# Performance work log

Hardware: AMD Instinct MI355X
Metric: run time of the kernel (lower is better)

## Reference

```python
import jax, jax.numpy as jnp
import numpy as np

N_NODES = 50000
N_EDGES = 400000
LATENT = 128
HIDDEN = 512
N_HEADS = 2          # latent // 64, NodeAttn default num_heads
HEAD_DIM = LATENT // N_HEADS
N_GRAPHS = 500
LN_EPS = 1e-5


def setup_inputs() -> dict:
    key = jax.random.key(0)
    ks = jax.random.split(key, 24)
    s = 0.02
    inp = {
        "edges": jax.random.randint(ks[0], (2, N_EDGES), 0, N_NODES, dtype=jnp.int32),
        "node_feat": jax.random.normal(ks[1], (N_NODES, LATENT), jnp.float32),
        "edge_attr": jax.random.normal(ks[2], (N_EDGES, LATENT), jnp.float32),
        "u": jax.random.normal(ks[3], (N_GRAPHS, LATENT), jnp.float32),
        "num_nodes": jnp.full((N_GRAPHS,), N_NODES // N_GRAPHS, jnp.int32),
        # NodeAttn params (shared for sent/received calls, as in the module)
        "w1": jax.random.normal(ks[4], (3 * LATENT, LATENT), jnp.float32) * s,
        "b1": jnp.zeros((LATENT,), jnp.float32),
        "w2": jax.random.normal(ks[5], (N_HEADS, HEAD_DIM), jnp.float32) * s,
        "w3": jax.random.normal(ks[6], (2 * LATENT, LATENT), jnp.float32) * s,
        "b3": jnp.zeros((LATENT,), jnp.float32),
        # Encoder MLP: 4*latent -> hidden -> hidden -> latent, LN before ReLU
        "mw0": jax.random.normal(ks[7], (4 * LATENT, HIDDEN), jnp.float32) * s,
        "mb0": jnp.zeros((HIDDEN,), jnp.float32),
        "ls0": jnp.ones((HIDDEN,), jnp.float32),
        "lb0": jnp.zeros((HIDDEN,), jnp.float32),
        "mw1": jax.random.normal(ks[8], (HIDDEN, HIDDEN), jnp.float32) * s,
        "mb1": jnp.zeros((HIDDEN,), jnp.float32),
        "ls1": jnp.ones((HIDDEN,), jnp.float32),
        "lb1": jnp.zeros((HIDDEN,), jnp.float32),
        "mw2": jax.random.normal(ks[9], (HIDDEN, LATENT), jnp.float32) * s,
        "mb2": jnp.zeros((LATENT,), jnp.float32),
    }
    return inp


def _layer_norm(x, scale, bias):
    mu = jnp.mean(x, axis=-1, keepdims=True)
    var = jnp.mean(jnp.square(x - mu), axis=-1, keepdims=True)
    return (x - mu) * jax.lax.rsqrt(var + LN_EPS) * scale + bias


def _node_attn(q, k, ea, index, n_nodes, w1, b1, w2, w3, b3):
    # per-edge multi-head scores -> segment softmax over destination index -> scatter-add
    h = jax.nn.leaky_relu(jnp.concatenate([q, k, ea], axis=-1) @ w1 + b1, 0.2)
    h = h.reshape(-1, N_HEADS, HEAD_DIM)                    # [E, H, D]
    logits = jnp.einsum("ehd,hd->eh", h, w2)                 # [E, H]
    m = jax.ops.segment_max(logits, index, num_segments=n_nodes)
    m = jnp.where(jnp.isfinite(m), m, 0.0)                   # empty segments
    e = jnp.exp(logits - m[index])
    z = jax.ops.segment_sum(e, index, num_segments=n_nodes)
    alpha = e / (z[index] + 1e-16)                           # [E, H]
    v = (jnp.concatenate([k, ea], axis=-1) @ w3 + b3).reshape(-1, N_HEADS, HEAD_DIM)
    out = jax.ops.segment_sum(alpha[..., None] * v, index, num_segments=n_nodes)
    return out.reshape(n_nodes, LATENT)


def reference(edges, node_feat, edge_attr, u, num_nodes, w1, b1, w2, w3, b3,
              mw0, mb0, ls0, lb0, mw1, mb1, ls1, lb1, mw2, mb2):
    n = node_feat.shape[0]
    row, col = edges[0], edges[1]
    sent = _node_attn(node_feat[row], node_feat[col], edge_attr, row, n, w1, b1, w2, w3, b3)
    recv = _node_attn(node_feat[col], node_feat[row], edge_attr, col, n, w1, b1, w2, w3, b3)
    glob = jnp.repeat(u, num_nodes, axis=0, total_repeat_length=n)
    x = jnp.concatenate([node_feat, sent, recv, glob], axis=1)   # [N, 4*latent]
    h = jax.nn.relu(_layer_norm(x @ mw0 + mb0, ls0, lb0))
    h = jax.nn.relu(_layer_norm(h @ mw1 + mb1, ls1, lb1))
    return h @ mw2 + mb2
```

## Files before the change

### kernel.cpp

```cpp
#include <hip/hip_runtime.h>
#include <math.h>

#define LATENT 128

typedef __attribute__((ext_vector_type(8))) short bf16x8;
typedef __attribute__((ext_vector_type(4))) float f32x4;
typedef __attribute__((ext_vector_type(2))) float f32x2;
typedef __attribute__((ext_vector_type(2))) int i32x2;
typedef __attribute__((ext_vector_type(2))) unsigned u32x2;
typedef __attribute__((ext_vector_type(4))) unsigned u32x4;

union U4B { uint4 u; bf16x8 v; };

template <typename T>
__device__ __forceinline__ T ntl(const T* p) { return __builtin_nontemporal_load(p); }

__device__ __forceinline__ unsigned short f2bf(float f) {
    unsigned int x = __float_as_uint(f);
    unsigned int r = (x + 0x7fffu + ((x >> 16) & 1u)) >> 16;
    return (unsigned short)r;
}
__device__ __forceinline__ float bf2f(unsigned short h) {
    return __uint_as_float(((unsigned int)h) << 16);
}
__device__ __forceinline__ unsigned pk2(float a, float b) {
    return (unsigned)f2bf(a) | ((unsigned)f2bf(b) << 16);
}

__device__ __forceinline__ void gld16(const void* g, void* l) {
    __builtin_amdgcn_global_load_lds(
        (const __attribute__((address_space(1))) unsigned int*)g,
        (__attribute__((address_space(3))) unsigned int*)l, 16, 0, 0);
}

__global__ void k_gid(const int* __restrict__ num_nodes, int G, int n, int* __restrict__ gid) {
    __shared__ int goff[1025];
    if (threadIdx.x == 0) {
        int acc = 0;
        for (int g = 0; g < G; ++g) { goff[g] = acc; acc += num_nodes[g]; }
        goff[G] = acc;
    }
    __syncthreads();
    for (int g = 0; g < G; ++g) {
        int s = goff[g];
        int e = goff[g + 1]; if (e > n) e = n;
        for (int i = s + (int)threadIdx.x; i < e; i += blockDim.x) gid[i] = g;
    }
}

#define FN  1152
#define FE3 1248
#define FEV 1280
__global__ __launch_bounds__(256) void k_pack2(const float* __restrict__ mw0,
                                               const float* __restrict__ mw1,
                                               const float* __restrict__ mw2,
                                               const float* __restrict__ w1,
                                               const float* __restrict__ w3,
                                               uint4* __restrict__ pw) {
    int tid = blockIdx.x * 256 + threadIdx.x;
    if (tid >= 1312 * 64) return;
    int fid = tid >> 6, lane = tid & 63;
    const float* src; int kt, nt, N;
    if (fid < 512)       { src = mw0;            kt = fid >> 5;           nt = fid & 31;           N = 512; }
    else if (fid < 1024) { src = mw1;            kt = (fid - 512) >> 5;   nt = (fid - 512) & 31;   N = 512; }
    else if (fid < 1152) { src = mw2;            kt = (fid - 1024) >> 3;  nt = (fid - 1024) & 7;   N = 128; }
    else if (fid < 1184) { src = w1;             kt = (fid - 1152) >> 3;  nt = (fid - 1152) & 7;   N = 128; }
    else if (fid < 1216) { src = w1 + 128 * 128; kt = (fid - 1184) >> 3;  nt = (fid - 1184) & 7;   N = 128; }
    else if (fid < 1248) { src = w3;             kt = (fid - 1216) >> 3;  nt = (fid - 1216) & 7;   N = 128; }
    else if (fid < 1280) { src = w1 + 256 * 128; kt = (fid - 1248) >> 3;  nt = (fid - 1248) & 7;   N = 128; }
    else                 { src = w3 + 128 * 128; kt = (fid - 1280) >> 3;  nt = (fid - 1280) & 7;   N = 128; }
    int col = nt * 16 + (lane & 15);
    int k0 = kt * 32 + (lane >> 4) * 8;
    unsigned int w[4];
#pragma unroll
    for (int p = 0; p < 4; ++p) {
        unsigned int lo = f2bf(src[(size_t)(k0 + 2 * p) * N + col]);
        unsigned int hi = f2bf(src[(size_t)(k0 + 2 * p + 1) * N + col]);
        w[p] = lo | (hi << 16);
    }
    pw[(size_t)fid * 64 + lane] = make_uint4(w[0], w[1], w[2], w[3]);
}

__global__ void k_count(const int* __restrict__ edges, int E,
                        int* __restrict__ deg_s, int* __restrict__ deg_r) {
    int e = blockIdx.x * 256 + threadIdx.x;
    if (e < E) { atomicAdd(&deg_s[edges[e]], 1); atomicAdd(&deg_r[edges[E + e]], 1); }
}

__global__ __launch_bounds__(1024) void k_scan(const int* __restrict__ deg, int n,
                                               int* __restrict__ rowptr, int* __restrict__ cursor) {
    __shared__ int wsum[16];
    int t = threadIdx.x;
    int chunk = (n + 1023) / 1024;
    int s = t * chunk; if (s > n) s = n;
    int epos = s + chunk; if (epos > n) epos = n;
    int sum = 0;
    for (int i = s; i < epos; ++i) sum += deg[i];
    int lane = t & 63, wid = t >> 6;
    int v = sum;
#pragma unroll
    for (int d = 1; d < 64; d <<= 1) { int o = __shfl_up(v, d); if (lane >= d) v += o; }
    if (lane == 63) wsum[wid] = v;
    __syncthreads();
    if (t < 16) {
        int wv = wsum[t];
#pragma unroll
        for (int d = 1; d < 16; d <<= 1) { int o = __shfl_up(wv, d, 16); if (t >= d) wv += o; }
        wsum[t] = wv;
    }
    __syncthreads();
    int woff = wid ? wsum[wid - 1] : 0;
    int run = v + woff - sum;
    for (int i = s; i < epos; ++i) { rowptr[i] = run; cursor[i] = run; run += deg[i]; }
    if (t == 1023) rowptr[n] = run;
}

__global__ void k_fill(const int* __restrict__ edges, int E,
                       int* __restrict__ cur_s, int* __restrict__ cur_r,
                       int* __restrict__ os_s, int* __restrict__ os_r,
                       int* __restrict__ sm_s, int* __restrict__ sm_r) {
    int e = blockIdx.x * 256 + threadIdx.x;
    if (e < E) {
        int r = edges[e], c = edges[E + e];
        int p = atomicAdd(&cur_s[r], 1); os_s[p] = c; sm_s[e] = p;
        int q = atomicAdd(&cur_r[c], 1); os_r[q] = r; sm_r[e] = q;
    }
}

__global__ __launch_bounds__(512) void k_nodepre2(const float* __restrict__ nf, int n,
                                                  const uint4* __restrict__ pw,
                                                  unsigned short* __restrict__ PQK,
                                                  unsigned short* __restrict__ PVh) {
    __shared__ uint4 xs[32 * 64];
    int t = threadIdx.x, lane = t & 63, w = t >> 6;
    int wr = w >> 2, wc = w & 3, l15 = lane & 15, lg = lane >> 4;
    int base = blockIdx.x * 128;
#pragma unroll
    for (int it = 0; it < 4; ++it) {
        int chunk = t + it * 512;
        int row = chunk >> 4, k8 = chunk & 15, k = k8 * 8;
        int node = base + row;
        f32x4 v0 = (f32x4)(0.f), v1 = (f32x4)(0.f);
        if (node < n) {
            const f32x4* s4 = (const f32x4*)(nf + (size_t)node * 128 + k);
            v0 = ntl(s4); v1 = ntl(s4 + 1);
        }
        uint4 pkv;
        pkv.x = pk2(v0.x, v0.y); pkv.y = pk2(v0.z, v0.w);
        pkv.z = pk2(v1.x, v1.y); pkv.w = pk2(v1.z, v1.w);
        int kt = k >> 5, g = (k >> 3) & 3;
        xs[(kt * 8 + (row >> 4)) * 64 + g * 16 + (row & 15)] = pkv;
    }
    __syncthreads();
    f32x4 acc[4][6];
#pragma unroll
    for (int rt = 0; rt < 4; ++rt)
#pragma unroll
        for (int ct = 0; ct < 6; ++ct) acc[rt][ct] = (f32x4)(0.f);
    for (int kt = 0; kt < 4; ++kt) {
        U4B a[4];
#pragma unroll
        for (int rt = 0; rt < 4; ++rt) a[rt].u = xs[(kt * 8 + wr * 4 + rt) * 64 + lane];
        U4B b[6];
#pragma unroll
        for (int ct = 0; ct < 6; ++ct) {
            int nt = wc * 6 + ct;
            int mat = nt >> 3, ntm = nt & 7;
            b[ct].u = pw[(size_t)(FN + mat * 32 + kt * 8 + ntm) * 64 + lane];
        }
#pragma unroll
        for (int rt = 0; rt < 4; ++rt)
#pragma unroll
            for (int ct = 0; ct < 6; ++ct)
                acc[rt][ct] = __builtin_amdgcn_mfma_f32_16x16x32_bf16(a[rt].v, b[ct].v, acc[rt][ct], 0, 0, 0);
    }
#pragma unroll
    for (int rt = 0; rt < 4; ++rt)
#pragma unroll
        for (int ct = 0; ct < 6; ++ct) {
            int nt = wc * 6 + ct;
#pragma unroll
            for (int reg = 0; reg < 4; ++reg) {
                int node = base + (wr * 4 + rt) * 16 + lg * 4 + reg;
                if (node < n) {
                    unsigned short hv = f2bf(acc[rt][ct][reg]);
                    if (nt < 16) PQK[(size_t)node * 256 + nt * 16 + l15] = hv;
                    else         PVh[(size_t)node * 128 + (nt - 16) * 16 + l15] = hv;
                }
            }
        }
}

__global__ __launch_bounds__(256) void k_eproj1(const int* __restrict__ edges,
                                                const float* __restrict__ ea, int E,
                                                const uint4* __restrict__ pw,
                                                const unsigned short* __restrict__ PQK,
                                                const float* __restrict__ b1,
                                                const float* __restrict__ w2,
                                                const int* __restrict__ sm_s,
                                                const int* __restrict__ sm_r,
                                                unsigned short* __restrict__ EVs,
                                                unsigned short* __restrict__ EVr,
                                                float* __restrict__ ess2, float* __restrict__ ers2) {
    __shared__ uint4 xs[16 * 64];
    __shared__ unsigned short edata[64 * 128];
    __shared__ unsigned short evdata[64 * 128];
    int t = threadIdx.x, lane = t & 63, w = t >> 6;
    int wc = w, l15 = lane & 15, lg = lane >> 4;
    int base = blockIdx.x * 64;
#pragma unroll
    for (int it = 0; it < 4; ++it) {
        int chunk = t + it * 256;
        int row = chunk >> 4, k8 = chunk & 15, k = k8 * 8;
        int e = base + row;
        f32x4 v0 = (f32x4)(0.f), v1 = (f32x4)(0.f);
        if (e < E) {
            const f32x4* s4 = (const f32x4*)(ea + (size_t)e * 128 + k);
            v0 = ntl(s4); v1 = ntl(s4 + 1);
        }
        uint4 pkv;
        pkv.x = pk2(v0.x, v0.y); pkv.y = pk2(v0.z, v0.w);
        pkv.z = pk2(v1.x, v1.y); pkv.w = pk2(v1.z, v1.w);
        int kt = k >> 5, g = (k >> 3) & 3;
        xs[(kt * 4 + (row >> 4)) * 64 + g * 16 + (row & 15)] = pkv;
    }
    __syncthreads();
    f32x4 acc[4][4];
#pragma unroll
    for (int rt = 0; rt < 4; ++rt)
#pragma unroll
        for (int ct = 0; ct < 4; ++ct) acc[rt][ct] = (f32x4)(0.f);
    for (int kt = 0; kt < 4; ++kt) {
        U4B a[4];
#pragma unroll
        for (int rt = 0; rt < 4; ++rt) a[rt].u = xs[(kt * 4 + rt) * 64 + lane];
        U4B b[4];
        b[0].u = pw[(size_t)(FE3 + kt * 8 + wc * 2 + 0) * 64 + lane];
        b[1].u = pw[(size_t)(FE3 + kt * 8 + wc * 2 + 1) * 64 + lane];
        b[2].u = pw[(size_t)(FEV + kt * 8 + wc * 2 + 0) * 64 + lane];
        b[3].u = pw[(size_t)(FEV + kt * 8 + wc * 2 + 1) * 64 + lane];
#pragma unroll
        for (int rt = 0; rt < 4; ++rt)
#pragma unroll
            for (int ct = 0; ct < 4; ++ct)
                acc[rt][ct] = __builtin_amdgcn_mfma_f32_16x16x32_bf16(a[rt].v, b[ct].v, acc[rt][ct], 0, 0, 0);
    }
#pragma unroll
    for (int rt = 0; rt < 4; ++rt)
#pragma unroll
        for (int cc = 0; cc < 2; ++cc) {
            int col = (wc * 2 + cc) * 16 + l15;
#pragma unroll
            for (int reg = 0; reg < 4; ++reg) {
                int e_loc = rt * 16 + lg * 4 + reg;
                edata[e_loc * 128 + col]  = f2bf(acc[rt][cc][reg]);
                evdata[e_loc * 128 + col] = f2bf(acc[rt][2 + cc][reg]);
            }
        }
    __syncthreads();
    {
        int e4 = lane >> 4, piece = lane & 15;
#pragma unroll
        for (int i = 0; i < 4; ++i) {
            int e_loc = w * 16 + i * 4 + e4;
            int e = base + e_loc;
            if (e < E) {
                u32x4 v = *(const u32x4*)&evdata[e_loc * 128 + piece * 8];
                __builtin_nontemporal_store(v, (u32x4*)(EVs + (size_t)sm_s[e] * 128 + piece * 8));
                __builtin_nontemporal_store(v, (u32x4*)(EVr + (size_t)sm_r[e] * 128 + piece * 8));
            }
        }
    }
    int esub = lane >> 3, dg = lane & 7;
    float b1r[16], w2r[16];
    {
        const float4* b4 = (const float4*)(b1 + dg * 16);
        const float4* w4 = (const float4*)(w2 + (dg >> 2) * 64 + (dg & 3) * 16);
#pragma unroll
        for (int q = 0; q < 4; ++q) {
            float4 bv = b4[q], wv = w4[q];
            b1r[q * 4 + 0] = bv.x; b1r[q * 4 + 1] = bv.y; b1r[q * 4 + 2] = bv.z; b1r[q * 4 + 3] = bv.w;
            w2r[q * 4 + 0] = wv.x; w2r[q * 4 + 1] = wv.y; w2r[q * 4 + 2] = wv.z; w2r[q * 4 + 3] = wv.w;
        }
    }
#pragma unroll
    for (int it = 0; it < 2; ++it) {
        int e_loc = w * 16 + it * 8 + esub;
        int e = base + e_loc;
        if (e >= E) break;
        int r = edges[e], c = edges[E + e];
        const uint4* Aqr = (const uint4*)(PQK + ((size_t)r << 8) + dg * 16);
        const uint4* Akc = (const uint4*)(PQK + ((size_t)c << 8) + 128 + dg * 16);
        const uint4* Aqc = (const uint4*)(PQK + ((size_t)c << 8) + dg * 16);
        const uint4* Akr = (const uint4*)(PQK + ((size_t)r << 8) + 128 + dg * 16);
        const uint4* Ae3 = (const uint4*)(&edata[e_loc * 128 + dg * 16]);
        float ps = 0.f, pr = 0.f;
#pragma unroll
        for (int half = 0; half < 2; ++half) {
            uint4 uqr = Aqr[half], ukc = Akc[half], uqc = Aqc[half], ukr = Akr[half], ue3 = Ae3[half];
            unsigned wqr[4] = {uqr.x, uqr.y, uqr.z, uqr.w};
            unsigned wkc[4] = {ukc.x, ukc.y, ukc.z, ukc.w};
            unsigned wqc[4] = {uqc.x, uqc.y, uqc.z, uqc.w};
            unsigned wkr[4] = {ukr.x, ukr.y, ukr.z, ukr.w};
            unsigned we3[4] = {ue3.x, ue3.y, ue3.z, ue3.w};
#pragma unroll
            for (int q = 0; q < 4; ++q) {
#pragma unroll
                for (int hl = 0; hl < 2; ++hl) {
                    int i = half * 8 + q * 2 + hl;
                    float fqr = hl ? __uint_as_float(wqr[q] & 0xffff0000u) : __uint_as_float(wqr[q] << 16);
                    float fkc = hl ? __uint_as_float(wkc[q] & 0xffff0000u) : __uint_as_float(wkc[q] << 16);
                    float fqc = hl ? __uint_as_float(wqc[q] & 0xffff0000u) : __uint_as_float(wqc[q] << 16);
                    float fkr = hl ? __uint_as_float(wkr[q] & 0xffff0000u) : __uint_as_float(wkr[q] << 16);
                    float fe3 = hl ? __uint_as_float(we3[q] & 0xffff0000u) : __uint_as_float(we3[q] << 16);
                    float com = fe3 + b1r[i];
                    float hs = fqr + fkc + com; hs = hs > 0.f ? hs : 0.2f * hs;
                    float hr = fqc + fkr + com; hr = hr > 0.f ? hr : 0.2f * hr;
                    ps += hs * w2r[i]; pr += hr * w2r[i];
                }
            }
        }
        ps += __shfl_xor(ps, 1); ps += __shfl_xor(ps, 2);
        pr += __shfl_xor(pr, 1); pr += __shfl_xor(pr, 2);
        float Es = expf(ps), Er = expf(pr);
        if (dg == 0) {
            __builtin_nontemporal_store(Es, &ess2[(size_t)sm_s[e] * 2]);
            __builtin_nontemporal_store(Er, &ers2[(size_t)sm_r[e] * 2]);
        } else if (dg == 4) {
            __builtin_nontemporal_store(Es, &ess2[(size_t)sm_s[e] * 2 + 1]);
            __builtin_nontemporal_store(Er, &ers2[(size_t)sm_r[e] * 2 + 1]);
        }
    }
}

__global__ __launch_bounds__(256) void k_aggr(int n,
                                              const int* __restrict__ rps, const int* __restrict__ os_s,
                                              const int* __restrict__ rpr, const int* __restrict__ os_r,
                                              const float* __restrict__ ess2, const float* __restrict__ ers2,
                                              const unsigned short* __restrict__ PVh,
                                              const unsigned short* __restrict__ EVs,
                                              const unsigned short* __restrict__ EVr,
                                              const float* __restrict__ b3,
                                              unsigned short* __restrict__ out_sh,
                                              unsigned short* __restrict__ out_rh) {
    int w = threadIdx.x >> 6, lane = threadIdx.x & 63;
    int unit = blockIdx.x * 4 + w;
    if (unit >= 2 * n) return;
    bool sent = unit < n;
    int node = sent ? unit : unit - n;
    const int*   rp = sent ? rps : rpr;
    const int*   os = sent ? os_s : os_r;
    const float* ex = sent ? ess2 : ers2;
    const unsigned* EVx = (const unsigned*)(sent ? EVs : EVr);
    const unsigned* PV32 = (const unsigned*)PVh;
    int s0 = rp[node], s1 = rp[node + 1];
    float b3a = b3[2 * lane], b3b = b3[2 * lane + 1];
    float z0 = 0.f, z1 = 0.f, acca = 0.f, accb = 0.f;
    int j = s0;
    for (; j + 4 <= s1; j += 4) {
        int oth[4]; f32x2 ez[4]; unsigned ev[4], pv[4];
#pragma unroll
        for (int q = 0; q < 4; ++q) oth[q] = os[j + q];
#pragma unroll
        for (int q = 0; q < 4; ++q) ez[q] = ntl((const f32x2*)(ex + 2 * (j + q)));
#pragma unroll
        for (int q = 0; q < 4; ++q) ev[q] = ntl(EVx + (size_t)(j + q) * 64 + lane);
#pragma unroll
        for (int q = 0; q < 4; ++q) pv[q] = PV32[(size_t)oth[q] * 64 + lane];
#pragma unroll
        for (int q = 0; q < 4; ++q) {
            float va = __uint_as_float(ev[q] << 16) + __uint_as_float(pv[q] << 16) + b3a;
            float vb = __uint_as_float(ev[q] & 0xffff0000u) + __uint_as_float(pv[q] & 0xffff0000u) + b3b;
            z0 += ez[q].x; z1 += ez[q].y;
            float aw = (lane < 32) ? ez[q].x : ez[q].y;
            acca += aw * va; accb += aw * vb;
        }
    }
    for (; j < s1; ++j) {
        int oth = os[j];
        f32x2 ez = ntl((const f32x2*)(ex + 2 * j));
        unsigned ev = ntl(EVx + (size_t)j * 64 + lane);
        unsigned pv = PV32[(size_t)oth * 64 + lane];
        float va = __uint_as_float(ev << 16) + __uint_as_float(pv << 16) + b3a;
        float vb = __uint_as_float(ev & 0xffff0000u) + __uint_as_float(pv & 0xffff0000u) + b3b;
        z0 += ez.x; z1 += ez.y;
        float aw = (lane < 32) ? ez.x : ez.y;
        acca += aw * va; accb += aw * vb;
    }
    float zz = (lane < 32) ? z0 : z1;
    float rz = 1.f / (zz + 1e-16f);
    unsigned o = pk2(acca * rz, accb * rz);
    unsigned* outp = (unsigned*)(sent ? out_sh : out_rh);
    outp[(size_t)node * 64 + lane] = o;
}

__global__ __launch_bounds__(512) void k_mlp9(
    const float* __restrict__ nf, const unsigned short* __restrict__ out_sh,
    const unsigned short* __restrict__ out_rh,
    const float* __restrict__ u, const int* __restrict__ gid, int n,
    const uint4* __restrict__ pw,
    const float* __restrict__ mb0, const float* __restrict__ ls0, const float* __restrict__ lb0,
    const float* __restrict__ mb1, const float* __restrict__ ls1, const float* __restrict__ lb1,
    const float* __restrict__ mb2, float* __restrict__ out) {
    extern __shared__ char smem[];
    char* hx = smem;
    char* bb = smem + 65536;
    float2* red = (float2*)(smem + 131072);

    int t = threadIdx.x, lane = t & 63, w = t >> 6;
    int wr = w >> 2, wc = w & 3, l15 = lane & 15, lg = lane >> 4;
    int base = blockIdx.x * 64;

    auto stage32 = [&](int fragbase, int d) {
        const uint4* src = pw + (size_t)fragbase * 64;
        char* dst = bb + (size_t)d * 32768;
#pragma unroll
        for (int q = 0; q < 4; ++q)
            gld16(src + q * 512 + t, dst + ((size_t)q * 512 + t) * 16);
    };
    auto stage8 = [&](int fragbase, int d) {
        const uint4* src = pw + (size_t)fragbase * 64;
        char* dst = bb + (size_t)d * 32768;
        gld16(src + t, dst + (size_t)t * 16);
    };

    stage32(0, 0);
#pragma unroll
    for (int it = 0; it < 16; ++it) {
        int chunk = t + it * 512;
        int row = chunk >> 7, kq = chunk & 127;
        int k = kq * 4;
        int node = base + row;
        u32x2 p = (u32x2)(0u);
        if (node < n) {
            int kk = k & 127;
            if (k < 128) {
                f32x4 v = ntl((const f32x4*)(nf + (size_t)node * 128 + kk));
                p.x = pk2(v.x, v.y); p.y = pk2(v.z, v.w);
            } else if (k < 384) {
                const unsigned short* s = (k < 256 ? out_sh : out_rh) + (size_t)node * 128 + kk;
                p = ntl((const u32x2*)s);
            } else {
                f32x4 v = *(const f32x4*)(u + (size_t)gid[node] * 128 + kk);
                p.x = pk2(v.x, v.y); p.y = pk2(v.z, v.w);
            }
        }
        int addr = (row * 1024 + k * 2) ^ ((row & 7) << 4);
        *(u32x2*)(hx + addr) = p;
    }
    __syncthreads();

    f32x4 acc[2][8];
    int buf = 0;
#pragma unroll
    for (int layer = 0; layer < 2; ++layer) {
        const float* MB = layer ? mb1 : mb0;
        const float* LS = layer ? ls1 : ls0;
        const float* LB = layer ? lb1 : lb0;
        const int fbase = layer ? 512 : 0;
#pragma unroll
        for (int rt = 0; rt < 2; ++rt)
#pragma unroll
            for (int ct = 0; ct < 8; ++ct) acc[rt][ct] = (f32x4)(0.f);

        for (int kt = 0; kt < 16; ++kt) {
            if (kt < 15)            stage32(fbase + (kt + 1) * 32, buf ^ 1);
            else if (layer == 0)    stage32(512, buf ^ 1);
            else                    stage8(1024, buf ^ 1);
            U4B b[8];
#pragma unroll
            for (int ct = 0; ct < 8; ++ct)
                b[ct].u = *(const uint4*)(bb + (size_t)buf * 32768 + ((wc * 8 + ct) * 64 + lane) * 16);
            U4B a[2];
#pragma unroll
            for (int rt = 0; rt < 2; ++rt) {
                int row = wr * 32 + rt * 16 + l15;
                int addr = (row * 1024 + kt * 64 + lg * 16) ^ ((row & 7) << 4);
                a[rt].u = *(const uint4*)(hx + addr);
            }
            __builtin_amdgcn_s_setprio(1);
#pragma unroll
            for (int rt = 0; rt < 2; ++rt)
#pragma unroll
                for (int ct = 0; ct < 8; ++ct)
                    acc[rt][ct] = __builtin_amdgcn_mfma_f32_16x16x32_bf16(a[rt].v, b[ct].v, acc[rt][ct], 0, 0, 0);
            __builtin_amdgcn_s_setprio(0);
            __syncthreads();
            buf ^= 1;
        }

        float mbv[8], lsv[8], lbv[8];
#pragma unroll
        for (int ct = 0; ct < 8; ++ct) {
            int col = wc * 128 + ct * 16 + l15;
            mbv[ct] = MB[col]; lsv[ct] = LS[col]; lbv[ct] = LB[col];
        }
#pragma unroll
        for (int rt = 0; rt < 2; ++rt)
#pragma unroll
            for (int reg = 0; reg < 4; ++reg) {
                float p = 0.f, q = 0.f;
#pragma unroll
                for (int ct = 0; ct < 8; ++ct) {
                    float y = acc[rt][ct][reg] + mbv[ct];
                    acc[rt][ct][reg] = y;
                    p += y; q += y * y;
                }
#pragma unroll
                for (int d = 1; d < 16; d <<= 1) { p += __shfl_xor(p, d); q += __shfl_xor(q, d); }
                if (l15 == 0) {
                    int row = wr * 32 + rt * 16 + lg * 4 + reg;
                    red[row * 4 + wc] = make_float2(p, q);
                }
            }
        __syncthreads();
#pragma unroll
        for (int rt = 0; rt < 2; ++rt)
#pragma unroll
            for (int reg = 0; reg < 4; ++reg) {
                int row = wr * 32 + rt * 16 + lg * 4 + reg;
                float2 r0 = red[row * 4 + 0], r1 = red[row * 4 + 1];
                float2 r2 = red[row * 4 + 2], r3 = red[row * 4 + 3];
                float S = r0.x + r1.x + r2.x + r3.x;
                float S2 = r0.y + r1.y + r2.y + r3.y;
                float mu = S * (1.f / 512.f);
                float var = S2 * (1.f / 512.f) - mu * mu;
                float rs = rsqrtf(var + 1e-5f);
                int rswz = (row & 7) << 4;
#pragma unroll
                for (int ct = 0; ct < 8; ++ct) {
                    float h = (acc[rt][ct][reg] - mu) * rs * lsv[ct] + lbv[ct];
                    h = fmaxf(h, 0.f);
                    int col = wc * 128 + ct * 16 + l15;
                    int addr = (row * 1024 + col * 2) ^ rswz;
                    *(unsigned short*)(hx + addr) = f2bf(h);
                }
            }
        __syncthreads();
    }

    f32x4 a2[2][2];
#pragma unroll
    for (int rt = 0; rt < 2; ++rt)
#pragma unroll
        for (int ct = 0; ct < 2; ++ct) a2[rt][ct] = (f32x4)(0.f);
    for (int kt = 0; kt < 16; ++kt) {
        if (kt < 15) stage8(1024 + (kt + 1) * 8, buf ^ 1);
        U4B b[2];
#pragma unroll
        for (int ct = 0; ct < 2; ++ct)
            b[ct].u = *(const uint4*)(bb + (size_t)buf * 32768 + ((wc * 2 + ct) * 64 + lane) * 16);
        U4B a[2];
#pragma unroll
        for (int rt = 0; rt < 2; ++rt) {
            int row = wr * 32 + rt * 16 + l15;
            int addr = (row * 1024 + kt * 64 + lg * 16) ^ ((row & 7) << 4);
            a[rt].u = *(const uint4*)(hx + addr);
        }
        __builtin_amdgcn_s_setprio(1);
#pragma unroll
        for (int rt = 0; rt < 2; ++rt)
#pragma unroll
            for (int ct = 0; ct < 2; ++ct)
                a2[rt][ct] = __builtin_amdgcn_mfma_f32_16x16x32_bf16(a[rt].v, b[ct].v, a2[rt][ct], 0, 0, 0);
        __builtin_amdgcn_s_setprio(0);
        __syncthreads();
        buf ^= 1;
    }
    float mb2v[2];
#pragma unroll
    for (int ct = 0; ct < 2; ++ct) mb2v[ct] = mb2[wc * 32 + ct * 16 + l15];
#pragma unroll
    for (int rt = 0; rt < 2; ++rt)
#pragma unroll
        for (int reg = 0; reg < 4; ++reg) {
            int node = base + wr * 32 + rt * 16 + lg * 4 + reg;
            if (node < n) {
#pragma unroll
                for (int ct = 0; ct < 2; ++ct)
                    __builtin_nontemporal_store(a2[rt][ct][reg] + mb2v[ct],
                        &out[(size_t)node * 128 + wc * 32 + ct * 16 + l15]);
            }
        }
}

extern "C" void kernel_launch(void* const* d_in, const int* in_sizes, int n_in,
                              void* d_out, int out_size, void* d_ws, size_t ws_size,
                              hipStream_t stream) {
    const int*   edges     = (const int*)d_in[0];
    const float* nf        = (const float*)d_in[1];
    const float* ea        = (const float*)d_in[2];
    const float* u         = (const float*)d_in[3];
    const int*   num_nodes = (const int*)d_in[4];
    const float* w1  = (const float*)d_in[5];
    const float* b1  = (const float*)d_in[6];
    const float* w2  = (const float*)d_in[7];
    const float* w3  = (const float*)d_in[8];
    const float* b3  = (const float*)d_in[9];
    const float* mw0 = (const float*)d_in[10];
    const float* mb0 = (const float*)d_in[11];
    const float* ls0 = (const float*)d_in[12];
    const float* lb0 = (const float*)d_in[13];
    const float* mw1 = (const float*)d_in[14];
    const float* mb1 = (const float*)d_in[15];
    const float* ls1 = (const float*)d_in[16];
    const float* lb1 = (const float*)d_in[17];
    const float* mw2 = (const float*)d_in[18];
    const float* mb2 = (const float*)d_in[19];

    int E = in_sizes[0] / 2;
    int n = in_sizes[1] / LATENT;
    int G = in_sizes[4];
    float* out = (float*)d_out;

    char* wsb = (char*)d_ws;
    size_t off = 0;
    auto alloc = [&](size_t bytes) { void* p = (void*)(wsb + off); off += (bytes + 15) & ~(size_t)15; return p; };
    uint4*          pw     = (uint4*)alloc((size_t)1312 * 64 * 16);
    unsigned short* PQK    = (unsigned short*)alloc((size_t)n * 256 * 2);
    unsigned short* PVh    = (unsigned short*)alloc((size_t)n * 128 * 2);
    unsigned short* EVs    = (unsigned short*)alloc((size_t)E * 128 * 2);
    unsigned short* EVr    = (unsigned short*)alloc((size_t)E * 128 * 2);
    float*          ess2   = (float*)alloc((size_t)E * 2 * 4);
    float*          ers2   = (float*)alloc((size_t)E * 2 * 4);
    unsigned short* out_sh = (unsigned short*)alloc((size_t)n * 128 * 2);
    unsigned short* out_rh = (unsigned short*)alloc((size_t)n * 128 * 2);
    int*            gid    = (int*)alloc((size_t)n * 4);
    int*            deg_s  = (int*)alloc((size_t)n * 4);
    int*            deg_r  = (int*)alloc((size_t)n * 4);
    int*            cur_s  = (int*)alloc((size_t)n * 4);
    int*            cur_r  = (int*)alloc((size_t)n * 4);
    int*            rps    = (int*)alloc((size_t)(n + 1) * 4);
    int*            rpr    = (int*)alloc((size_t)(n + 1) * 4);
    int*            os_s   = (int*)alloc((size_t)E * 4);
    int*            os_r   = (int*)alloc((size_t)E * 4);
    int*            sm_s   = (int*)alloc((size_t)E * 4);
    int*            sm_r   = (int*)alloc((size_t)E * 4);

    hipMemsetAsync(deg_s, 0, (size_t)2 * n * 4 + 16, stream);

    hipFuncSetAttribute((const void*)k_mlp9, hipFuncAttributeMaxDynamicSharedMemorySize, 133120);

    k_gid<<<1, 256, 0, stream>>>(num_nodes, G, n, gid);
    k_pack2<<<(1312 * 64 + 255) / 256, 256, 0, stream>>>(mw0, mw1, mw2, w1, w3, pw);
    k_count<<<(E + 255) / 256, 256, 0, stream>>>(edges, E, deg_s, deg_r);
    k_scan<<<1, 1024, 0, stream>>>(deg_s, n, rps, cur_s);
    k_scan<<<1, 1024, 0, stream>>>(deg_r, n, rpr, cur_r);
    k_fill<<<(E + 255) / 256, 256, 0, stream>>>(edges, E, cur_s, cur_r, os_s, os_r, sm_s, sm_r);
    k_nodepre2<<<(n + 127) / 128, 512, 0, stream>>>(nf, n, pw, PQK, PVh);
    k_eproj1<<<(E + 63) / 64, 256, 0, stream>>>(edges, ea, E, pw, PQK, b1, w2, sm_s, sm_r,
                                                EVs, EVr, ess2, ers2);
    k_aggr<<<(2 * n + 3) / 4, 256, 0, stream>>>(n, rps, os_s, rpr, os_r,
                                                ess2, ers2, PVh, EVs, EVr, b3, out_sh, out_rh);
    k_mlp9<<<(n + 63) / 64, 512, 133120, stream>>>(nf, out_sh, out_rh, u, gid, n, pw,
                                                   mb0, ls0, lb0, mb1, ls1, lb1, mb2, out);
}
```

Before: 842.8 us.

## Halve MLP tile to 32 rows and single-buffer weight staging

The fused node MLP kernel now processes 32 nodes per block with 4 waves instead of 64 nodes with 8 waves. The weight staging buffer drops from double to single buffering, with an extra barrier so loads into LDS are issued after the fragments are read. LDS use per block halves, which should let more blocks sit on each CU. In exchange, each block re-reads all weights for half as many rows, and overlap between weight loads and MFMA within a block shrinks.

```diff
diff --git a/kernel.cpp b/kernel.cpp
--- a/kernel.cpp
+++ b/kernel.cpp
@@ -394,7 +394,7 @@
     outp[(size_t)node * 64 + lane] = o;
 }
 
-__global__ __launch_bounds__(512) void k_mlp9(
+__global__ __launch_bounds__(256) void k_mlp10(
     const float* __restrict__ nf, const unsigned short* __restrict__ out_sh,
     const unsigned short* __restrict__ out_rh,
     const float* __restrict__ u, const int* __restrict__ gid, int n,
@@ -404,30 +404,30 @@
     const float* __restrict__ mb2, float* __restrict__ out) {
     extern __shared__ char smem[];
     char* hx = smem;
-    char* bb = smem + 65536;
-    float2* red = (float2*)(smem + 131072);
-
-    int t = threadIdx.x, lane = t & 63, w = t >> 6;
-    int wr = w >> 2, wc = w & 3, l15 = lane & 15, lg = lane >> 4;
-    int base = blockIdx.x * 64;
-
-    auto stage32 = [&](int fragbase, int d) {
+    char* bb = smem + 32768;
+    float2* red = (float2*)(smem + 65536);
+
+    int t = threadIdx.x, lane = t & 63, wc = t >> 6;
+    int l15 = lane & 15, lg = lane >> 4;
+    int base = blockIdx.x * 32;
+
+    auto stage32 = [&](int fragbase) {
         const uint4* src = pw + (size_t)fragbase * 64;
-        char* dst = bb + (size_t)d * 32768;
-#pragma unroll
-        for (int q = 0; q < 4; ++q)
-            gld16(src + q * 512 + t, dst + ((size_t)q * 512 + t) * 16);
+#pragma unroll
+        for (int q = 0; q < 8; ++q)
+            gld16(src + q * 256 + t, bb + ((size_t)q * 256 + t) * 16);
     };
-    auto stage8 = [&](int fragbase, int d) {
+    auto stage8 = [&](int fragbase) {
         const uint4* src = pw + (size_t)fragbase * 64;
-        char* dst = bb + (size_t)d * 32768;
-        gld16(src + t, dst + (size_t)t * 16);
+#pragma unroll
+        for (int q = 0; q < 2; ++q)
+            gld16(src + q * 256 + t, bb + ((size_t)q * 256 + t) * 16);
     };
 
-    stage32(0, 0);
+    stage32(0);
 #pragma unroll
     for (int it = 0; it < 16; ++it) {
-        int chunk = t + it * 512;
+        int chunk = t + it * 256;
         int row = chunk >> 7, kq = chunk & 127;
         int k = kq * 4;
         int node = base + row;
@@ -451,7 +451,6 @@
     __syncthreads();
 
     f32x4 acc[2][8];
-    int buf = 0;
 #pragma unroll
     for (int layer = 0; layer < 2; ++layer) {
         const float* MB = layer ? mb1 : mb0;
@@ -464,20 +463,21 @@
             for (int ct = 0; ct < 8; ++ct) acc[rt][ct] = (f32x4)(0.f);
 
         for (int kt = 0; kt < 16; ++kt) {
-            if (kt < 15)            stage32(fbase + (kt + 1) * 32, buf ^ 1);
-            else if (layer == 0)    stage32(512, buf ^ 1);
-            else                    stage8(1024, buf ^ 1);
             U4B b[8];
 #pragma unroll
             for (int ct = 0; ct < 8; ++ct)
-                b[ct].u = *(const uint4*)(bb + (size_t)buf * 32768 + ((wc * 8 + ct) * 64 + lane) * 16);
+                b[ct].u = *(const uint4*)(bb + (((size_t)wc * 8 + ct) * 64 + lane) * 16);
             U4B a[2];
 #pragma unroll
             for (int rt = 0; rt < 2; ++rt) {
-                int row = wr * 32 + rt * 16 + l15;
+                int row = rt * 16 + l15;
                 int addr = (row * 1024 + kt * 64 + lg * 16) ^ ((row & 7) << 4);
                 a[rt].u = *(const uint4*)(hx + addr);
             }
+            __syncthreads();
+            if (kt < 15)            stage32(fbase + (kt + 1) * 32);
+            else if (layer == 0)    stage32(512);
+            else                    stage8(1024);
             __builtin_amdgcn_s_setprio(1);
 #pragma unroll
             for (int rt = 0; rt < 2; ++rt)
@@ -486,7 +486,6 @@
                     acc[rt][ct] = __builtin_amdgcn_mfma_f32_16x16x32_bf16(a[rt].v, b[ct].v, acc[rt][ct], 0, 0, 0);
             __builtin_amdgcn_s_setprio(0);
             __syncthreads();
-            buf ^= 1;
         }
 
         float mbv[8], lsv[8], lbv[8];
@@ -509,7 +508,7 @@
 #pragma unroll
                 for (int d = 1; d < 16; d <<= 1) { p += __shfl_xor(p, d); q += __shfl_xor(q, d); }
                 if (l15 == 0) {
-                    int row = wr * 32 + rt * 16 + lg * 4 + reg;
+                    int row = rt * 16 + lg * 4 + reg;
                     red[row * 4 + wc] = make_float2(p, q);
                 }
             }
@@ -518,7 +517,7 @@
         for (int rt = 0; rt < 2; ++rt)
 #pragma unroll
             for (int reg = 0; reg < 4; ++reg) {
-                int row = wr * 32 + rt * 16 + lg * 4 + reg;
+                int row = rt * 16 + lg * 4 + reg;
                 float2 r0 = red[row * 4 + 0], r1 = red[row * 4 + 1];
                 float2 r2 = red[row * 4 + 2], r3 = red[row * 4 + 3];
                 float S = r0.x + r1.x + r2.x + r3.x;
@@ -545,18 +544,19 @@
 #pragma unroll
         for (int ct = 0; ct < 2; ++ct) a2[rt][ct] = (f32x4)(0.f);
     for (int kt = 0; kt < 16; ++kt) {
-        if (kt < 15) stage8(1024 + (kt + 1) * 8, buf ^ 1);
         U4B b[2];
 #pragma unroll
         for (int ct = 0; ct < 2; ++ct)
-            b[ct].u = *(const uint4*)(bb + (size_t)buf * 32768 + ((wc * 2 + ct) * 64 + lane) * 16);
+            b[ct].u = *(const uint4*)(bb + (((size_t)wc * 2 + ct) * 64 + lane) * 16);
         U4B a[2];
 #pragma unroll
         for (int rt = 0; rt < 2; ++rt) {
-            int row = wr * 32 + rt * 16 + l15;
+            int row = rt * 16 + l15;
             int addr = (row * 1024 + kt * 64 + lg * 16) ^ ((row & 7) << 4);
             a[rt].u = *(const uint4*)(hx + addr);
         }
+        __syncthreads();
+        if (kt < 15) stage8(1024 + (kt + 1) * 8);
         __builtin_amdgcn_s_setprio(1);
 #pragma unroll
         for (int rt = 0; rt < 2; ++rt)
@@ -565,7 +565,6 @@
                 a2[rt][ct] = __builtin_amdgcn_mfma_f32_16x16x32_bf16(a[rt].v, b[ct].v, a2[rt][ct], 0, 0, 0);
         __builtin_amdgcn_s_setprio(0);
         __syncthreads();
-        buf ^= 1;
     }
     float mb2v[2];
 #pragma unroll
@@ -574,7 +573,7 @@
     for (int rt = 0; rt < 2; ++rt)
 #pragma unroll
         for (int reg = 0; reg < 4; ++reg) {
-            int node = base + wr * 32 + rt * 16 + lg * 4 + reg;
+            int node = base + rt * 16 + lg * 4 + reg;
             if (node < n) {
 #pragma unroll
                 for (int ct = 0; ct < 2; ++ct)
@@ -639,7 +638,7 @@
 
     hipMemsetAsync(deg_s, 0, (size_t)2 * n * 4 + 16, stream);
 
-    hipFuncSetAttribute((const void*)k_mlp9, hipFuncAttributeMaxDynamicSharedMemorySize, 133120);
+    hipFuncSetAttribute((const void*)k_mlp10, hipFuncAttributeMaxDynamicSharedMemorySize, 66560);
 
     k_gid<<<1, 256, 0, stream>>>(num_nodes, G, n, gid);
     k_pack2<<<(1312 * 64 + 255) / 256, 256, 0, stream>>>(mw0, mw1, mw2, w1, w3, pw);
@@ -652,6 +651,6 @@
                                                 EVs, EVr, ess2, ers2);
     k_aggr<<<(2 * n + 3) / 4, 256, 0, stream>>>(n, rps, os_s, rpr, os_r,
                                                 ess2, ers2, PVh, EVs, EVr, b3, out_sh, out_rh);
-    k_mlp9<<<(n + 63) / 64, 512, 133120, stream>>>(nf, out_sh, out_rh, u, gid, n, pw,
+    k_mlp10<<<(n + 31) / 32, 256, 66560, stream>>>(nf, out_sh, out_rh, u, gid, n, pw,
                                                    mb0, ls0, lb0, mb1, ls1, lb1, mb2, out);
 }
```

New measurement: 920.9 us. 9.3% more time.

## Load MLP weight fragments directly from global memory instead of LDS double-buffer

Applied to the files above, without the earlier changes.

The fused MLP kernel no longer stages weight fragments into a double-buffered LDS region with global_load_lds and per-k-step barriers. Each wave now reads its B fragments straight from global memory (L2-resident packed weights), which drops the per-iteration __syncthreads. This halves dynamic shared memory to about 66 KB and adds a launch-bounds occupancy hint, so more blocks can be resident per CU. The cost is more global/L2 traffic, since the four row-group waves each fetch the same fragments, and the loads are no longer prefetched a step ahead.

```diff
diff --git a/kernel.cpp b/kernel.cpp
--- a/kernel.cpp
+++ b/kernel.cpp
@@ -25,12 +25,6 @@
 }
 __device__ __forceinline__ unsigned pk2(float a, float b) {
     return (unsigned)f2bf(a) | ((unsigned)f2bf(b) << 16);
-}
-
-__device__ __forceinline__ void gld16(const void* g, void* l) {
-    __builtin_amdgcn_global_load_lds(
-        (const __attribute__((address_space(1))) unsigned int*)g,
-        (__attribute__((address_space(3))) unsigned int*)l, 16, 0, 0);
 }
 
 __global__ void k_gid(const int* __restrict__ num_nodes, int G, int n, int* __restrict__ gid) {
@@ -394,7 +388,7 @@
     outp[(size_t)node * 64 + lane] = o;
 }
 
-__global__ __launch_bounds__(512) void k_mlp9(
+__global__ __launch_bounds__(512, 4) void k_mlp11(
     const float* __restrict__ nf, const unsigned short* __restrict__ out_sh,
     const unsigned short* __restrict__ out_rh,
     const float* __restrict__ u, const int* __restrict__ gid, int n,
@@ -404,27 +398,12 @@
     const float* __restrict__ mb2, float* __restrict__ out) {
     extern __shared__ char smem[];
     char* hx = smem;
-    char* bb = smem + 65536;
-    float2* red = (float2*)(smem + 131072);
+    float2* red = (float2*)(smem + 65536);
 
     int t = threadIdx.x, lane = t & 63, w = t >> 6;
     int wr = w >> 2, wc = w & 3, l15 = lane & 15, lg = lane >> 4;
     int base = blockIdx.x * 64;
 
-    auto stage32 = [&](int fragbase, int d) {
-        const uint4* src = pw + (size_t)fragbase * 64;
-        char* dst = bb + (size_t)d * 32768;
-#pragma unroll
-        for (int q = 0; q < 4; ++q)
-            gld16(src + q * 512 + t, dst + ((size_t)q * 512 + t) * 16);
-    };
-    auto stage8 = [&](int fragbase, int d) {
-        const uint4* src = pw + (size_t)fragbase * 64;
-        char* dst = bb + (size_t)d * 32768;
-        gld16(src + t, dst + (size_t)t * 16);
-    };
-
-    stage32(0, 0);
 #pragma unroll
     for (int it = 0; it < 16; ++it) {
         int chunk = t + it * 512;
@@ -451,26 +430,18 @@
     __syncthreads();
 
     f32x4 acc[2][8];
-    int buf = 0;
 #pragma unroll
     for (int layer = 0; layer < 2; ++layer) {
         const float* MB = layer ? mb1 : mb0;
         const float* LS = layer ? ls1 : ls0;
         const float* LB = layer ? lb1 : lb0;
-        const int fbase = layer ? 512 : 0;
+        const uint4* PW = pw + ((size_t)(layer ? 512 : 0) + wc * 8) * 64 + lane;
 #pragma unroll
         for (int rt = 0; rt < 2; ++rt)
 #pragma unroll
             for (int ct = 0; ct < 8; ++ct) acc[rt][ct] = (f32x4)(0.f);
 
         for (int kt = 0; kt < 16; ++kt) {
-            if (kt < 15)            stage32(fbase + (kt + 1) * 32, buf ^ 1);
-            else if (layer == 0)    stage32(512, buf ^ 1);
-            else                    stage8(1024, buf ^ 1);
-            U4B b[8];
-#pragma unroll
-            for (int ct = 0; ct < 8; ++ct)
-                b[ct].u = *(const uint4*)(bb + (size_t)buf * 32768 + ((wc * 8 + ct) * 64 + lane) * 16);
             U4B a[2];
 #pragma unroll
             for (int rt = 0; rt < 2; ++rt) {
@@ -478,15 +449,19 @@
                 int addr = (row * 1024 + kt * 64 + lg * 16) ^ ((row & 7) << 4);
                 a[rt].u = *(const uint4*)(hx + addr);
             }
-            __builtin_amdgcn_s_setprio(1);
-#pragma unroll
-            for (int rt = 0; rt < 2; ++rt)
-#pragma unroll
-                for (int ct = 0; ct < 8; ++ct)
-                    acc[rt][ct] = __builtin_amdgcn_mfma_f32_16x16x32_bf16(a[rt].v, b[ct].v, acc[rt][ct], 0, 0, 0);
-            __builtin_amdgcn_s_setprio(0);
-            __syncthreads();
-            buf ^= 1;
+#pragma unroll
+            for (int h = 0; h < 2; ++h) {
+                U4B b[4];
+#pragma unroll
+                for (int ct = 0; ct < 4; ++ct)
+                    b[ct].u = PW[(size_t)(kt * 32 + h * 4 + ct) * 64];
+#pragma unroll
+                for (int rt = 0; rt < 2; ++rt)
+#pragma unroll
+                    for (int ct = 0; ct < 4; ++ct)
+                        acc[rt][h * 4 + ct] = __builtin_amdgcn_mfma_f32_16x16x32_bf16(
+                            a[rt].v, b[ct].v, acc[rt][h * 4 + ct], 0, 0, 0);
+            }
         }
 
         float mbv[8], lsv[8], lbv[8];
@@ -544,28 +519,25 @@
     for (int rt = 0; rt < 2; ++rt)
 #pragma unroll
         for (int ct = 0; ct < 2; ++ct) a2[rt][ct] = (f32x4)(0.f);
-    for (int kt = 0; kt < 16; ++kt) {
-        if (kt < 15) stage8(1024 + (kt + 1) * 8, buf ^ 1);
-        U4B b[2];
-#pragma unroll
-        for (int ct = 0; ct < 2; ++ct)
-            b[ct].u = *(const uint4*)(bb + (size_t)buf * 32768 + ((wc * 2 + ct) * 64 + lane) * 16);
-        U4B a[2];
-#pragma unroll
-        for (int rt = 0; rt < 2; ++rt) {
-            int row = wr * 32 + rt * 16 + l15;
-            int addr = (row * 1024 + kt * 64 + lg * 16) ^ ((row & 7) << 4);
-            a[rt].u = *(const uint4*)(hx + addr);
-        }
-        __builtin_amdgcn_s_setprio(1);
-#pragma unroll
-        for (int rt = 0; rt < 2; ++rt)
+    {
+        const uint4* PW2 = pw + ((size_t)1024 + wc * 2) * 64 + lane;
+        for (int kt = 0; kt < 16; ++kt) {
+            U4B a[2], b[2];
+#pragma unroll
+            for (int rt = 0; rt < 2; ++rt) {
+                int row = wr * 32 + rt * 16 + l15;
+                int addr = (row * 1024 + kt * 64 + lg * 16) ^ ((row & 7) << 4);
+                a[rt].u = *(const uint4*)(hx + addr);
+            }
 #pragma unroll
             for (int ct = 0; ct < 2; ++ct)
-                a2[rt][ct] = __builtin_amdgcn_mfma_f32_16x16x32_bf16(a[rt].v, b[ct].v, a2[rt][ct], 0, 0, 0);
-        __builtin_amdgcn_s_setprio(0);
-        __syncthreads();
-        buf ^= 1;
+                b[ct].u = PW2[(size_t)(kt * 8 + ct) * 64];
+#pragma unroll
+            for (int rt = 0; rt < 2; ++rt)
+#pragma unroll
+                for (int ct = 0; ct < 2; ++ct)
+                    a2[rt][ct] = __builtin_amdgcn_mfma_f32_16x16x32_bf16(a[rt].v, b[ct].v, a2[rt][ct], 0, 0, 0);
+        }
     }
     float mb2v[2];
 #pragma unroll
@@ -639,7 +611,7 @@
 
     hipMemsetAsync(deg_s, 0, (size_t)2 * n * 4 + 16, stream);
 
-    hipFuncSetAttribute((const void*)k_mlp9, hipFuncAttributeMaxDynamicSharedMemorySize, 133120);
+    hipFuncSetAttribute((const void*)k_mlp11, hipFuncAttributeMaxDynamicSharedMemorySize, 67584);
 
     k_gid<<<1, 256, 0, stream>>>(num_nodes, G, n, gid);
     k_pack2<<<(1312 * 64 + 255) / 256, 256, 0, stream>>>(mw0, mw1, mw2, w1, w3, pw);
@@ -652,6 +624,6 @@
                                                 EVs, EVr, ess2, ers2);
     k_aggr<<<(2 * n + 3) / 4, 256, 0, stream>>>(n, rps, os_s, rpr, os_r,
                                                 ess2, ers2, PVh, EVs, EVr, b3, out_sh, out_rh);
-    k_mlp9<<<(n + 63) / 64, 512, 133120, stream>>>(nf, out_sh, out_rh, u, gid, n, pw,
+    k_mlp11<<<(n + 63) / 64, 512, 67584, stream>>>(nf, out_sh, out_rh, u, gid, n, pw,
                                                    mb0, ls0, lb0, mb1, ls1, lb1, mb2, out);
 }
```

New measurement: 890.9 us. 1.06x slower.
